# Kernel tuning notes

Measured on AMD Instinct MI355X. Metric: run time of the kernel, lower is better.

## Reference

```python
import jax, jax.numpy as jnp
import numpy as np

BS, N, C = 16, 128, 512
EPS = 1e-5


def setup_inputs() -> dict:
    key = jax.random.key(0)
    ks = jax.random.split(key, 6)
    x = jax.random.normal(ks[0], (BS, N, C), dtype=jnp.float32)
    y = jax.random.normal(ks[1], (BS, C), dtype=jnp.float32)
    # edge conv: Conv2d(2C -> 1, 1x1), init std sqrt(2/(1*1*1))
    conv_e_w = jax.random.normal(ks[2], (1, 2 * C), dtype=jnp.float32) * np.sqrt(2.0)
    conv_e_b = jnp.zeros((1,), dtype=jnp.float32)
    bn_e_g = jnp.ones((1,), dtype=jnp.float32)
    bn_e_b = jnp.zeros((1,), dtype=jnp.float32)
    bn_e_m = jnp.zeros((1,), dtype=jnp.float32)
    bn_e_v = jnp.ones((1,), dtype=jnp.float32)
    # feature conv: Conv2d(2C -> C, 1x1), init std sqrt(2/C)
    conv_f_w = jax.random.normal(ks[3], (C, 2 * C), dtype=jnp.float32) * np.sqrt(2.0 / C)
    conv_f_b = jnp.zeros((C,), dtype=jnp.float32)
    bn_f_g = jnp.ones((C,), dtype=jnp.float32)
    bn_f_b = jnp.zeros((C,), dtype=jnp.float32)
    bn_f_m = jnp.zeros((C,), dtype=jnp.float32)
    bn_f_v = jnp.ones((C,), dtype=jnp.float32)
    return {
        "x": x, "y": y,
        "conv_e_w": conv_e_w, "conv_e_b": conv_e_b,
        "bn_e_g": bn_e_g, "bn_e_b": bn_e_b, "bn_e_m": bn_e_m, "bn_e_v": bn_e_v,
        "conv_f_w": conv_f_w, "conv_f_b": conv_f_b,
        "bn_f_g": bn_f_g, "bn_f_b": bn_f_b, "bn_f_m": bn_f_m, "bn_f_v": bn_f_v,
    }


def reference(x, y, conv_e_w, conv_e_b, bn_e_g, bn_e_b, bn_e_m, bn_e_v,
              conv_f_w, conv_f_b, bn_f_g, bn_f_b, bn_f_m, bn_f_v):
    bs, n, c = x.shape
    # ---- Wcompute: pairwise |x_i - x_j| -> conv1x1(2C->1) + BN + mask + softmax ----
    diff = jnp.abs(x[:, :, None, :] - x[:, None, :, :])  # [bs, N, N, C]
    w_diff = conv_e_w[0, :c]   # weights on pairwise-diff channels
    w_y = conv_e_w[0, c:]      # weights on broadcast y channels
    # 1x1 conv collapses to einsum; y part is constant over (i, j)
    score = (jnp.einsum('bijc,c->bij', diff, w_diff)
             + (y @ w_y)[:, None, None] + conv_e_b[0])  # [bs, N, N]
    # BatchNorm2d(1), inference mode
    score = (score - bn_e_m[0]) * (bn_e_g[0] * jax.lax.rsqrt(bn_e_v[0] + EPS)) + bn_e_b[0]
    # mask diagonal (W_id * 1e8) then softmax over neighbors j
    score = score - jnp.eye(n, dtype=score.dtype)[None] * 1e8
    W = jax.nn.softmax(score, axis=2)  # [bs, N, N]
    # ---- Gconv: neighbor aggregation + conv1x1(2C->C) + BN + ReLU ----
    x_nb = jnp.einsum('bij,bjc->bic', W, x)       # [bs, N, C]
    h = jnp.concatenate([x, x_nb], axis=2)        # [bs, N, 2C]
    out = jnp.einsum('bnk,ck->bnc', h, conv_f_w) + conv_f_b  # [bs, N, C]
    # BatchNorm2d(C), inference mode (per-channel)
    out = (out - bn_f_m) * (bn_f_g * jax.lax.rsqrt(bn_f_v + EPS)) + bn_f_b
    return jax.nn.relu(out)
```

## Files before the change

kernel.cpp:

```cpp
#include <hip/hip_runtime.h>
#include <hip/hip_bf16.h>

#define BSZ  16
#define NTOK 128
#define CHN  512
#define KTOT 1024
#define EPSV 1e-5f

typedef __attribute__((ext_vector_type(8))) short bf16x8;
typedef __attribute__((ext_vector_type(4))) float f32x4;

union BfPack4 { ushort4 u; __hip_bfloat16 h[4]; };

__global__ __launch_bounds__(128)
void k1_score_softmax_xnb(const float* __restrict__ xg,
                          const float* __restrict__ wde,
                          const float* __restrict__ bn_e_g,
                          const float* __restrict__ bn_e_v,
                          const float* __restrict__ wf,
                          __hip_bfloat16* __restrict__ hb,
                          __hip_bfloat16* __restrict__ wfb)
{
    __shared__ float xs[64][129];
    __shared__ float wrow[4][132];
    __shared__ float red[2][8];

    const int t   = threadIdx.x;
    const int blk = blockIdx.x;
    const int b   = blk >> 5;
    const int i0  = (blk & 31) << 2;
    const float* __restrict__ xb = xg + (size_t)b * NTOK * CHN;

    {
        const float* wr = wf + (size_t)blk * KTOT;
        float4 u0 = *(const float4*)&wr[t * 8];
        float4 u1 = *(const float4*)&wr[t * 8 + 4];
        BfPack4 p0, p1;
        p0.h[0] = __float2bfloat16(u0.x); p0.h[1] = __float2bfloat16(u0.y);
        p0.h[2] = __float2bfloat16(u0.z); p0.h[3] = __float2bfloat16(u0.w);
        p1.h[0] = __float2bfloat16(u1.x); p1.h[1] = __float2bfloat16(u1.y);
        p1.h[2] = __float2bfloat16(u1.z); p1.h[3] = __float2bfloat16(u1.w);
        *(ushort4*)&wfb[(size_t)blk * KTOT + t * 8]     = p0.u;
        *(ushort4*)&wfb[(size_t)blk * KTOT + t * 8 + 4] = p1.u;
    }

    float acc[4] = {0.f, 0.f, 0.f, 0.f};

    for (int c0 = 0; c0 < CHN; c0 += 64) {
        #pragma unroll
        for (int p = 0; p < 16; ++p) {
            const int j  = p * 8 + (t >> 4);
            const int c4 = (t & 15) * 4;
            float4 v = *(const float4*)&xb[(size_t)j * CHN + c0 + c4];
            xs[c4 + 0][j] = v.x; xs[c4 + 1][j] = v.y;
            xs[c4 + 2][j] = v.z; xs[c4 + 3][j] = v.w;
        }
        __syncthreads();

        #pragma unroll 4
        for (int g4 = 0; g4 < 16; ++g4) {
            const int c = c0 + g4 * 4;
            const float4 wdv = *(const float4*)&wde[c];
            const float4 xi0 = *(const float4*)&xb[(size_t)(i0 + 0) * CHN + c];
            const float4 xi1 = *(const float4*)&xb[(size_t)(i0 + 1) * CHN + c];
            const float4 xi2 = *(const float4*)&xb[(size_t)(i0 + 2) * CHN + c];
            const float4 xi3 = *(const float4*)&xb[(size_t)(i0 + 3) * CHN + c];
            const int cl = g4 * 4;
            const float xj0 = xs[cl + 0][t];
            const float xj1 = xs[cl + 1][t];
            const float xj2 = xs[cl + 2][t];
            const float xj3 = xs[cl + 3][t];
            acc[0] += fabsf(xi0.x - xj0) * wdv.x + fabsf(xi0.y - xj1) * wdv.y
                    + fabsf(xi0.z - xj2) * wdv.z + fabsf(xi0.w - xj3) * wdv.w;
            acc[1] += fabsf(xi1.x - xj0) * wdv.x + fabsf(xi1.y - xj1) * wdv.y
                    + fabsf(xi1.z - xj2) * wdv.z + fabsf(xi1.w - xj3) * wdv.w;
            acc[2] += fabsf(xi2.x - xj0) * wdv.x + fabsf(xi2.y - xj1) * wdv.y
                    + fabsf(xi2.z - xj2) * wdv.z + fabsf(xi2.w - xj3) * wdv.w;
            acc[3] += fabsf(xi3.x - xj0) * wdv.x + fabsf(xi3.y - xj1) * wdv.y
                    + fabsf(xi3.z - xj2) * wdv.z + fabsf(xi3.w - xj3) * wdv.w;
        }
        __syncthreads();
    }

    const float sc = bn_e_g[0] * rsqrtf(bn_e_v[0] + EPSV);
    float logit[4];
    #pragma unroll
    for (int ti = 0; ti < 4; ++ti) {
        logit[ti] = acc[ti] * sc;
        if (t == i0 + ti) logit[ti] -= 1e8f;
    }
    const int wid = t >> 6, lane = t & 63;
    float mx[4];
    #pragma unroll
    for (int ti = 0; ti < 4; ++ti) {
        float v = logit[ti];
        #pragma unroll
        for (int off = 32; off > 0; off >>= 1) v = fmaxf(v, __shfl_xor(v, off));
        mx[ti] = v;
    }
    if (lane == 0) {
        red[wid][0] = mx[0]; red[wid][1] = mx[1];
        red[wid][2] = mx[2]; red[wid][3] = mx[3];
    }
    __syncthreads();
    float pe[4], sm[4];
    #pragma unroll
    for (int ti = 0; ti < 4; ++ti) {
        const float M = fmaxf(red[0][ti], red[1][ti]);
        pe[ti] = __expf(logit[ti] - M);
        float v = pe[ti];
        #pragma unroll
        for (int off = 32; off > 0; off >>= 1) v += __shfl_xor(v, off);
        sm[ti] = v;
    }
    if (lane == 0) {
        red[wid][4] = sm[0]; red[wid][5] = sm[1];
        red[wid][6] = sm[2]; red[wid][7] = sm[3];
    }
    __syncthreads();
    #pragma unroll
    for (int ti = 0; ti < 4; ++ti) {
        const float S = red[0][4 + ti] + red[1][4 + ti];
        wrow[ti][t] = pe[ti] / S;
    }
    __syncthreads();

    const int c4 = t << 2;
    float4 av[4];
    #pragma unroll
    for (int ti = 0; ti < 4; ++ti) { av[ti].x = av[ti].y = av[ti].z = av[ti].w = 0.f; }

    for (int j = 0; j < NTOK; ++j) {
        const float4 xj = *(const float4*)&xb[(size_t)j * CHN + c4];
        const float w0 = wrow[0][j], w1 = wrow[1][j], w2 = wrow[2][j], w3 = wrow[3][j];
        av[0].x += w0 * xj.x; av[0].y += w0 * xj.y; av[0].z += w0 * xj.z; av[0].w += w0 * xj.w;
        av[1].x += w1 * xj.x; av[1].y += w1 * xj.y; av[1].z += w1 * xj.z; av[1].w += w1 * xj.w;
        av[2].x += w2 * xj.x; av[2].y += w2 * xj.y; av[2].z += w2 * xj.z; av[2].w += w2 * xj.w;
        av[3].x += w3 * xj.x; av[3].y += w3 * xj.y; av[3].z += w3 * xj.z; av[3].w += w3 * xj.w;
    }

    #pragma unroll
    for (int ti = 0; ti < 4; ++ti) {
        const size_t row = (size_t)(b * NTOK + i0 + ti);
        BfPack4 pk;
        pk.h[0] = __float2bfloat16(av[ti].x); pk.h[1] = __float2bfloat16(av[ti].y);
        pk.h[2] = __float2bfloat16(av[ti].z); pk.h[3] = __float2bfloat16(av[ti].w);
        *(ushort4*)&hb[row * KTOT + CHN + c4] = pk.u;
        const float4 xv = *(const float4*)&xb[(size_t)(i0 + ti) * CHN + c4];
        pk.h[0] = __float2bfloat16(xv.x); pk.h[1] = __float2bfloat16(xv.y);
        pk.h[2] = __float2bfloat16(xv.z); pk.h[3] = __float2bfloat16(xv.w);
        *(ushort4*)&hb[row * KTOT + c4] = pk.u;
    }
}

__global__ __launch_bounds__(256)
void k2_gemm_bn_relu(const __hip_bfloat16* __restrict__ hbp,
                     const __hip_bfloat16* __restrict__ wfbp,
                     const float* __restrict__ fb,
                     const float* __restrict__ gg,
                     const float* __restrict__ bb,
                     const float* __restrict__ mm,
                     const float* __restrict__ vv,
                     float* __restrict__ out)
{
    const int blk  = blockIdx.x;
    const int r0   = (blk >> 3) << 6;
    const int c0   = (blk & 7) << 6;
    const int t    = threadIdx.x;
    const int w    = t >> 6;
    const int lane = t & 63;
    const int wm   = w & 1;
    const int wn   = w >> 1;
    const int m16  = lane & 15;
    const int q    = lane >> 4;

    const short* A0 = (const short*)hbp  + (size_t)(r0 + wm * 32 + m16) * KTOT + q * 8;
    const short* B0 = (const short*)wfbp + (size_t)(c0 + wn * 32 + m16) * KTOT + q * 8;

    f32x4 acc00 = {0.f, 0.f, 0.f, 0.f};
    f32x4 acc01 = acc00, acc10 = acc00, acc11 = acc00;

    #pragma unroll 4
    for (int k0 = 0; k0 < KTOT; k0 += 32) {
        const bf16x8 aA = *(const bf16x8*)(A0 + k0);
        const bf16x8 aB = *(const bf16x8*)(A0 + 16 * KTOT + k0);
        const bf16x8 bA = *(const bf16x8*)(B0 + k0);
        const bf16x8 bB = *(const bf16x8*)(B0 + 16 * KTOT + k0);
        acc00 = __builtin_amdgcn_mfma_f32_16x16x32_bf16(aA, bA, acc00, 0, 0, 0);
        acc01 = __builtin_amdgcn_mfma_f32_16x16x32_bf16(aA, bB, acc01, 0, 0, 0);
        acc10 = __builtin_amdgcn_mfma_f32_16x16x32_bf16(aB, bA, acc10, 0, 0, 0);
        acc11 = __builtin_amdgcn_mfma_f32_16x16x32_bf16(aB, bB, acc11, 0, 0, 0);
    }

    #pragma unroll
    for (int ni = 0; ni < 2; ++ni) {
        const int c = c0 + wn * 32 + ni * 16 + m16;
        const float gf = gg[c] * rsqrtf(vv[c] + EPSV);
        const float ad = fb[c] - mm[c];
        const float bv = bb[c];
        const f32x4 acr0 = ni ? acc01 : acc00;
        const f32x4 acr1 = ni ? acc11 : acc10;
        #pragma unroll
        for (int r2 = 0; r2 < 4; ++r2) {
            int row = r0 + wm * 32 + q * 4 + r2;
            float val = (acr0[r2] + ad) * gf + bv;
            out[(size_t)row * CHN + c] = fmaxf(val, 0.f);
            row += 16;
            val = (acr1[r2] + ad) * gf + bv;
            out[(size_t)row * CHN + c] = fmaxf(val, 0.f);
        }
    }
}

extern "C" void kernel_launch(void* const* d_in, const int* in_sizes, int n_in,
                              void* d_out, int out_size, void* d_ws, size_t ws_size,
                              hipStream_t stream) {
    const float* x        = (const float*)d_in[0];
    const float* conv_e_w = (const float*)d_in[2];
    const float* bn_e_g   = (const float*)d_in[4];
    const float* bn_e_v   = (const float*)d_in[7];
    const float* conv_f_w = (const float*)d_in[8];
    const float* conv_f_b = (const float*)d_in[9];
    const float* bn_f_g   = (const float*)d_in[10];
    const float* bn_f_b   = (const float*)d_in[11];
    const float* bn_f_m   = (const float*)d_in[12];
    const float* bn_f_v   = (const float*)d_in[13];
    float* out = (float*)d_out;

    __hip_bfloat16* hb  = (__hip_bfloat16*)d_ws;
    __hip_bfloat16* wfb = hb + (size_t)2048 * 1024;

    k1_score_softmax_xnb<<<512, 128, 0, stream>>>(x, conv_e_w, bn_e_g, bn_e_v,
                                                  conv_f_w, hb, wfb);
    k2_gemm_bn_relu<<<256, 256, 0, stream>>>(hb, wfb, conv_f_b, bn_f_g, bn_f_b,
                                             bn_f_m, bn_f_v, out);
}
```

Measured before the change: 141.6 us.

## Split channel reduction across four thread groups in score kernel with 512 threads

The first kernel grows from 128 to 512 threads per block. The pairwise score reduction over channels is split into four channel quarters, each staged into its own shared-memory slab, and the partials are combined through shared memory before the softmax. The neighbor aggregation is likewise split over four j-quarters and summed through shared memory. This gives each block more waves to hide memory latency and shortens the serial loop per thread, at the cost of more shared memory, extra barriers and partial-sum traffic. The softmax section places __syncthreads calls inside divergent branches, with matching counts on each side.

After: 153.5 us. 8.4% more time.

```diff
diff --git a/kernel.cpp b/kernel.cpp
--- a/kernel.cpp
+++ b/kernel.cpp
@@ -7,12 +7,15 @@
 #define KTOT 1024
 #define EPSV 1e-5f
 
+#define LROW 132
+#define QS   (32 * LROW)
+
 typedef __attribute__((ext_vector_type(8))) short bf16x8;
 typedef __attribute__((ext_vector_type(4))) float f32x4;
 
 union BfPack4 { ushort4 u; __hip_bfloat16 h[4]; };
 
-__global__ __launch_bounds__(128)
+__global__ __launch_bounds__(512, 4)
 void k1_score_softmax_xnb(const float* __restrict__ xg,
                           const float* __restrict__ wde,
                           const float* __restrict__ bn_e_g,
@@ -21,9 +24,10 @@
                           __hip_bfloat16* __restrict__ hb,
                           __hip_bfloat16* __restrict__ wfb)
 {
-    __shared__ float xs[64][129];
-    __shared__ float wrow[4][132];
-    __shared__ float red[2][8];
+    __shared__ float smem[4 * QS];
+    __shared__ float part[4][4][128];
+    __shared__ float wrow[4][LROW];
+    __shared__ float red[16];
 
     const int t   = threadIdx.x;
     const int blk = blockIdx.x;
@@ -31,122 +35,154 @@
     const int i0  = (blk & 31) << 2;
     const float* __restrict__ xb = xg + (size_t)b * NTOK * CHN;
 
-    {
+    if (t < 256) {
         const float* wr = wf + (size_t)blk * KTOT;
-        float4 u0 = *(const float4*)&wr[t * 8];
-        float4 u1 = *(const float4*)&wr[t * 8 + 4];
-        BfPack4 p0, p1;
-        p0.h[0] = __float2bfloat16(u0.x); p0.h[1] = __float2bfloat16(u0.y);
-        p0.h[2] = __float2bfloat16(u0.z); p0.h[3] = __float2bfloat16(u0.w);
-        p1.h[0] = __float2bfloat16(u1.x); p1.h[1] = __float2bfloat16(u1.y);
-        p1.h[2] = __float2bfloat16(u1.z); p1.h[3] = __float2bfloat16(u1.w);
-        *(ushort4*)&wfb[(size_t)blk * KTOT + t * 8]     = p0.u;
-        *(ushort4*)&wfb[(size_t)blk * KTOT + t * 8 + 4] = p1.u;
-    }
-
+        float4 u = *(const float4*)&wr[t * 4];
+        BfPack4 p;
+        p.h[0] = __float2bfloat16(u.x); p.h[1] = __float2bfloat16(u.y);
+        p.h[2] = __float2bfloat16(u.z); p.h[3] = __float2bfloat16(u.w);
+        *(ushort4*)&wfb[(size_t)blk * KTOT + t * 4] = p.u;
+    }
+
+    const int j = t & 127;
+    const int q = t >> 7;
     float acc[4] = {0.f, 0.f, 0.f, 0.f};
 
-    for (int c0 = 0; c0 < CHN; c0 += 64) {
-        #pragma unroll
-        for (int p = 0; p < 16; ++p) {
-            const int j  = p * 8 + (t >> 4);
-            const int c4 = (t & 15) * 4;
-            float4 v = *(const float4*)&xb[(size_t)j * CHN + c0 + c4];
-            xs[c4 + 0][j] = v.x; xs[c4 + 1][j] = v.y;
-            xs[c4 + 2][j] = v.z; xs[c4 + 3][j] = v.w;
-        }
-        __syncthreads();
-
-        #pragma unroll 4
-        for (int g4 = 0; g4 < 16; ++g4) {
-            const int c = c0 + g4 * 4;
-            const float4 wdv = *(const float4*)&wde[c];
+    const int j_s = t >> 2;
+    const int lg  = t & 3;
+
+    for (int s = 0; s < 4; ++s) {
+        #pragma unroll
+        for (int g = 0; g < 8; ++g) {
+            const int G   = lg + 4 * g;
+            const int qq  = G >> 3;
+            const int idx = G & 7;
+            const int cg  = qq * 128 + s * 32 + idx * 4;
+            float4 v = *(const float4*)&xb[(size_t)j_s * CHN + cg];
+            float* dst = &smem[qq * QS + (idx * 4) * LROW + j_s];
+            dst[0 * LROW] = v.x; dst[1 * LROW] = v.y;
+            dst[2 * LROW] = v.z; dst[3 * LROW] = v.w;
+        }
+        __syncthreads();
+
+        const int cbase = q * 128 + s * 32;
+        #pragma unroll
+        for (int g = 0; g < 8; ++g) {
+            const int c = cbase + g * 4;
+            const float4 wd  = *(const float4*)&wde[c];
             const float4 xi0 = *(const float4*)&xb[(size_t)(i0 + 0) * CHN + c];
             const float4 xi1 = *(const float4*)&xb[(size_t)(i0 + 1) * CHN + c];
             const float4 xi2 = *(const float4*)&xb[(size_t)(i0 + 2) * CHN + c];
             const float4 xi3 = *(const float4*)&xb[(size_t)(i0 + 3) * CHN + c];
-            const int cl = g4 * 4;
-            const float xj0 = xs[cl + 0][t];
-            const float xj1 = xs[cl + 1][t];
-            const float xj2 = xs[cl + 2][t];
-            const float xj3 = xs[cl + 3][t];
-            acc[0] += fabsf(xi0.x - xj0) * wdv.x + fabsf(xi0.y - xj1) * wdv.y
-                    + fabsf(xi0.z - xj2) * wdv.z + fabsf(xi0.w - xj3) * wdv.w;
-            acc[1] += fabsf(xi1.x - xj0) * wdv.x + fabsf(xi1.y - xj1) * wdv.y
-                    + fabsf(xi1.z - xj2) * wdv.z + fabsf(xi1.w - xj3) * wdv.w;
-            acc[2] += fabsf(xi2.x - xj0) * wdv.x + fabsf(xi2.y - xj1) * wdv.y
-                    + fabsf(xi2.z - xj2) * wdv.z + fabsf(xi2.w - xj3) * wdv.w;
-            acc[3] += fabsf(xi3.x - xj0) * wdv.x + fabsf(xi3.y - xj1) * wdv.y
-                    + fabsf(xi3.z - xj2) * wdv.z + fabsf(xi3.w - xj3) * wdv.w;
-        }
-        __syncthreads();
-    }
-
-    const float sc = bn_e_g[0] * rsqrtf(bn_e_v[0] + EPSV);
-    float logit[4];
-    #pragma unroll
-    for (int ti = 0; ti < 4; ++ti) {
-        logit[ti] = acc[ti] * sc;
-        if (t == i0 + ti) logit[ti] -= 1e8f;
-    }
-    const int wid = t >> 6, lane = t & 63;
-    float mx[4];
-    #pragma unroll
-    for (int ti = 0; ti < 4; ++ti) {
-        float v = logit[ti];
-        #pragma unroll
-        for (int off = 32; off > 0; off >>= 1) v = fmaxf(v, __shfl_xor(v, off));
-        mx[ti] = v;
-    }
-    if (lane == 0) {
-        red[wid][0] = mx[0]; red[wid][1] = mx[1];
-        red[wid][2] = mx[2]; red[wid][3] = mx[3];
-    }
+            const float* xr = &smem[q * QS + (g * 4) * LROW + j];
+            const float xj0 = xr[0 * LROW];
+            const float xj1 = xr[1 * LROW];
+            const float xj2 = xr[2 * LROW];
+            const float xj3 = xr[3 * LROW];
+            acc[0] += fabsf(xi0.x - xj0) * wd.x + fabsf(xi0.y - xj1) * wd.y
+                    + fabsf(xi0.z - xj2) * wd.z + fabsf(xi0.w - xj3) * wd.w;
+            acc[1] += fabsf(xi1.x - xj0) * wd.x + fabsf(xi1.y - xj1) * wd.y
+                    + fabsf(xi1.z - xj2) * wd.z + fabsf(xi1.w - xj3) * wd.w;
+            acc[2] += fabsf(xi2.x - xj0) * wd.x + fabsf(xi2.y - xj1) * wd.y
+                    + fabsf(xi2.z - xj2) * wd.z + fabsf(xi2.w - xj3) * wd.w;
+            acc[3] += fabsf(xi3.x - xj0) * wd.x + fabsf(xi3.y - xj1) * wd.y
+                    + fabsf(xi3.z - xj2) * wd.z + fabsf(xi3.w - xj3) * wd.w;
+        }
+        __syncthreads();
+    }
+
+    #pragma unroll
+    for (int ti = 0; ti < 4; ++ti) part[q][ti][j] = acc[ti];
     __syncthreads();
-    float pe[4], sm[4];
-    #pragma unroll
-    for (int ti = 0; ti < 4; ++ti) {
-        const float M = fmaxf(red[0][ti], red[1][ti]);
-        pe[ti] = __expf(logit[ti] - M);
-        float v = pe[ti];
-        #pragma unroll
-        for (int off = 32; off > 0; off >>= 1) v += __shfl_xor(v, off);
-        sm[ti] = v;
-    }
-    if (lane == 0) {
-        red[wid][4] = sm[0]; red[wid][5] = sm[1];
-        red[wid][6] = sm[2]; red[wid][7] = sm[3];
+
+    if (t < 128) {
+        const float sc = bn_e_g[0] * rsqrtf(bn_e_v[0] + EPSV);
+        float logit[4];
+        #pragma unroll
+        for (int ti = 0; ti < 4; ++ti) {
+            logit[ti] = (part[0][ti][t] + part[1][ti][t]
+                       + part[2][ti][t] + part[3][ti][t]) * sc;
+            if (t == i0 + ti) logit[ti] -= 1e8f;
+        }
+        const int wid = t >> 6, lane = t & 63;
+        float mx[4];
+        #pragma unroll
+        for (int ti = 0; ti < 4; ++ti) {
+            float v = logit[ti];
+            #pragma unroll
+            for (int off = 32; off > 0; off >>= 1) v = fmaxf(v, __shfl_xor(v, off));
+            mx[ti] = v;
+        }
+        if (lane == 0) {
+            red[wid * 8 + 0] = mx[0]; red[wid * 8 + 1] = mx[1];
+            red[wid * 8 + 2] = mx[2]; red[wid * 8 + 3] = mx[3];
+        }
+        __syncthreads();
+        float pe[4], sm[4];
+        #pragma unroll
+        for (int ti = 0; ti < 4; ++ti) {
+            const float M = fmaxf(red[ti], red[8 + ti]);
+            pe[ti] = __expf(logit[ti] - M);
+            float v = pe[ti];
+            #pragma unroll
+            for (int off = 32; off > 0; off >>= 1) v += __shfl_xor(v, off);
+            sm[ti] = v;
+        }
+        if (lane == 0) {
+            red[wid * 8 + 4] = sm[0]; red[wid * 8 + 5] = sm[1];
+            red[wid * 8 + 6] = sm[2]; red[wid * 8 + 7] = sm[3];
+        }
+        __syncthreads();
+        #pragma unroll
+        for (int ti = 0; ti < 4; ++ti) {
+            const float S = red[4 + ti] + red[12 + ti];
+            wrow[ti][t] = pe[ti] / S;
+        }
+    } else {
+        __syncthreads();
+        __syncthreads();
     }
     __syncthreads();
-    #pragma unroll
-    for (int ti = 0; ti < 4; ++ti) {
-        const float S = red[0][4 + ti] + red[1][4 + ti];
-        wrow[ti][t] = pe[ti] / S;
-    }
+
+    const int c4 = (t & 127) << 2;
+    const int jq = t >> 7;
+    float4 a2[4];
+    #pragma unroll
+    for (int ti = 0; ti < 4; ++ti) { a2[ti].x = a2[ti].y = a2[ti].z = a2[ti].w = 0.f; }
+
+    #pragma unroll 4
+    for (int jj = 0; jj < 32; ++jj) {
+        const int jx = jq * 32 + jj;
+        const float4 xj = *(const float4*)&xb[(size_t)jx * CHN + c4];
+        const float w0 = wrow[0][jx], w1 = wrow[1][jx];
+        const float w2 = wrow[2][jx], w3 = wrow[3][jx];
+        a2[0].x += w0 * xj.x; a2[0].y += w0 * xj.y; a2[0].z += w0 * xj.z; a2[0].w += w0 * xj.w;
+        a2[1].x += w1 * xj.x; a2[1].y += w1 * xj.y; a2[1].z += w1 * xj.z; a2[1].w += w1 * xj.w;
+        a2[2].x += w2 * xj.x; a2[2].y += w2 * xj.y; a2[2].z += w2 * xj.z; a2[2].w += w2 * xj.w;
+        a2[3].x += w3 * xj.x; a2[3].y += w3 * xj.y; a2[3].z += w3 * xj.z; a2[3].w += w3 * xj.w;
+    }
+    #pragma unroll
+    for (int ti = 0; ti < 4; ++ti)
+        *(float4*)&smem[(jq * 4 + ti) * CHN + c4] = a2[ti];
     __syncthreads();
 
-    const int c4 = t << 2;
-    float4 av[4];
-    #pragma unroll
-    for (int ti = 0; ti < 4; ++ti) { av[ti].x = av[ti].y = av[ti].z = av[ti].w = 0.f; }
-
-    for (int j = 0; j < NTOK; ++j) {
-        const float4 xj = *(const float4*)&xb[(size_t)j * CHN + c4];
-        const float w0 = wrow[0][j], w1 = wrow[1][j], w2 = wrow[2][j], w3 = wrow[3][j];
-        av[0].x += w0 * xj.x; av[0].y += w0 * xj.y; av[0].z += w0 * xj.z; av[0].w += w0 * xj.w;
-        av[1].x += w1 * xj.x; av[1].y += w1 * xj.y; av[1].z += w1 * xj.z; av[1].w += w1 * xj.w;
-        av[2].x += w2 * xj.x; av[2].y += w2 * xj.y; av[2].z += w2 * xj.z; av[2].w += w2 * xj.w;
-        av[3].x += w3 * xj.x; av[3].y += w3 * xj.y; av[3].z += w3 * xj.z; av[3].w += w3 * xj.w;
-    }
-
-    #pragma unroll
-    for (int ti = 0; ti < 4; ++ti) {
-        const size_t row = (size_t)(b * NTOK + i0 + ti);
+    {
+        const int ti2 = t >> 7;
+        float4 s0 = *(const float4*)&smem[(0 * 4 + ti2) * CHN + c4];
+        float4 s1 = *(const float4*)&smem[(1 * 4 + ti2) * CHN + c4];
+        float4 s2 = *(const float4*)&smem[(2 * 4 + ti2) * CHN + c4];
+        float4 s3 = *(const float4*)&smem[(3 * 4 + ti2) * CHN + c4];
+        float4 sum;
+        sum.x = s0.x + s1.x + s2.x + s3.x;
+        sum.y = s0.y + s1.y + s2.y + s3.y;
+        sum.z = s0.z + s1.z + s2.z + s3.z;
+        sum.w = s0.w + s1.w + s2.w + s3.w;
+        const size_t row = (size_t)(b * NTOK + i0 + ti2);
         BfPack4 pk;
-        pk.h[0] = __float2bfloat16(av[ti].x); pk.h[1] = __float2bfloat16(av[ti].y);
-        pk.h[2] = __float2bfloat16(av[ti].z); pk.h[3] = __float2bfloat16(av[ti].w);
+        pk.h[0] = __float2bfloat16(sum.x); pk.h[1] = __float2bfloat16(sum.y);
+        pk.h[2] = __float2bfloat16(sum.z); pk.h[3] = __float2bfloat16(sum.w);
         *(ushort4*)&hb[row * KTOT + CHN + c4] = pk.u;
-        const float4 xv = *(const float4*)&xb[(size_t)(i0 + ti) * CHN + c4];
+        const float4 xv = *(const float4*)&xb[(size_t)(i0 + ti2) * CHN + c4];
         pk.h[0] = __float2bfloat16(xv.x); pk.h[1] = __float2bfloat16(xv.y);
         pk.h[2] = __float2bfloat16(xv.z); pk.h[3] = __float2bfloat16(xv.w);
         *(ushort4*)&hb[row * KTOT + c4] = pk.u;
@@ -172,10 +208,10 @@
     const int wm   = w & 1;
     const int wn   = w >> 1;
     const int m16  = lane & 15;
-    const int q    = lane >> 4;
-
-    const short* A0 = (const short*)hbp  + (size_t)(r0 + wm * 32 + m16) * KTOT + q * 8;
-    const short* B0 = (const short*)wfbp + (size_t)(c0 + wn * 32 + m16) * KTOT + q * 8;
+    const int qq   = lane >> 4;
+
+    const short* A0 = (const short*)hbp  + (size_t)(r0 + wm * 32 + m16) * KTOT + qq * 8;
+    const short* B0 = (const short*)wfbp + (size_t)(c0 + wn * 32 + m16) * KTOT + qq * 8;
 
     f32x4 acc00 = {0.f, 0.f, 0.f, 0.f};
     f32x4 acc01 = acc00, acc10 = acc00, acc11 = acc00;
@@ -202,7 +238,7 @@
         const f32x4 acr1 = ni ? acc11 : acc10;
         #pragma unroll
         for (int r2 = 0; r2 < 4; ++r2) {
-            int row = r0 + wm * 32 + q * 4 + r2;
+            int row = r0 + wm * 32 + qq * 4 + r2;
             float val = (acr0[r2] + ad) * gf + bv;
             out[(size_t)row * CHN + c] = fmaxf(val, 0.f);
             row += 16;
@@ -230,7 +266,7 @@
     __hip_bfloat16* hb  = (__hip_bfloat16*)d_ws;
     __hip_bfloat16* wfb = hb + (size_t)2048 * 1024;
 
-    k1_score_softmax_xnb<<<512, 128, 0, stream>>>(x, conv_e_w, bn_e_g, bn_e_v,
+    k1_score_softmax_xnb<<<512, 512, 0, stream>>>(x, conv_e_w, bn_e_g, bn_e_v,
                                                   conv_f_w, hb, wfb);
     k2_gemm_bn_relu<<<256, 256, 0, stream>>>(hb, wfb, conv_f_b, bn_f_g, bn_f_b,
                                              bn_f_m, bn_f_v, out);
```

## Split score kernel into transpose, split-K scores, softmax, and MFMA aggregation

Applied to the files above, without the earlier changes.

Replaces the single fused score/softmax/aggregation kernel with four kernels. A transpose kernel writes x^T in fp32 and bf16. The pairwise score is split across 8 channel slices (4096 blocks) to raise parallelism, with partial sums written to a workspace and then reduced in a softmax kernel. The neighbor aggregation W·x now runs on MFMA in bf16. This adds extra launches, global round-trips for partial scores, and lower precision in W and x for the aggregation.

Result: faster. 123.1 us (median of 3 runs) (-13.1%).

```diff
diff --git a/kernel.cpp b/kernel.cpp
--- a/kernel.cpp
+++ b/kernel.cpp
@@ -1,7 +1,6 @@
 #include <hip/hip_runtime.h>
 #include <hip/hip_bf16.h>
 
-#define BSZ  16
 #define NTOK 128
 #define CHN  512
 #define KTOT 1024
@@ -12,144 +11,206 @@
 
 union BfPack4 { ushort4 u; __hip_bfloat16 h[4]; };
 
+
+__global__ __launch_bounds__(256)
+void k0_transpose(const float* __restrict__ xg,
+                  float* __restrict__ xT,
+                  __hip_bfloat16* __restrict__ xTbf,
+                  __hip_bfloat16* __restrict__ hb)
+{
+    __shared__ float ts[64 * 68];
+    const int t  = threadIdx.x;
+    const int bk = blockIdx.x;
+    const int b  = bk >> 4;
+    const int jt = (bk >> 3) & 1;
+    const int ct = bk & 7;
+    const int j0 = jt * 64, c0 = ct * 64;
+
+    const int jr = t >> 2, qd = t & 3;
+    const float* src = xg + ((size_t)(b * NTOK) + j0 + jr) * CHN + c0 + qd * 16;
+    float4 v0 = *(const float4*)&src[0];
+    float4 v1 = *(const float4*)&src[4];
+    float4 v2 = *(const float4*)&src[8];
+    float4 v3 = *(const float4*)&src[12];
+    *(float4*)&ts[jr * 68 + qd * 16 + 0]  = v0;
+    *(float4*)&ts[jr * 68 + qd * 16 + 4]  = v1;
+    *(float4*)&ts[jr * 68 + qd * 16 + 8]  = v2;
+    *(float4*)&ts[jr * 68 + qd * 16 + 12] = v3;
+
+    {
+        __hip_bfloat16* hrow = hb + ((size_t)(b * NTOK) + j0 + jr) * KTOT + c0 + qd * 16;
+        BfPack4 p;
+        p.h[0]=__float2bfloat16(v0.x); p.h[1]=__float2bfloat16(v0.y);
+        p.h[2]=__float2bfloat16(v0.z); p.h[3]=__float2bfloat16(v0.w);
+        *(ushort4*)&hrow[0] = p.u;
+        p.h[0]=__float2bfloat16(v1.x); p.h[1]=__float2bfloat16(v1.y);
+        p.h[2]=__float2bfloat16(v1.z); p.h[3]=__float2bfloat16(v1.w);
+        *(ushort4*)&hrow[4] = p.u;
+        p.h[0]=__float2bfloat16(v2.x); p.h[1]=__float2bfloat16(v2.y);
+        p.h[2]=__float2bfloat16(v2.z); p.h[3]=__float2bfloat16(v2.w);
+        *(ushort4*)&hrow[8] = p.u;
+        p.h[0]=__float2bfloat16(v3.x); p.h[1]=__float2bfloat16(v3.y);
+        p.h[2]=__float2bfloat16(v3.z); p.h[3]=__float2bfloat16(v3.w);
+        *(ushort4*)&hrow[12] = p.u;
+    }
+    __syncthreads();
+
+    const int cs = t >> 4, jj = (t & 15) * 4;
+    #pragma unroll
+    for (int m = 0; m < 4; ++m) {
+        const int c = cs + 16 * m;
+        float4 o;
+        o.x = ts[(jj + 0) * 68 + c];
+        o.y = ts[(jj + 1) * 68 + c];
+        o.z = ts[(jj + 2) * 68 + c];
+        o.w = ts[(jj + 3) * 68 + c];
+        const size_t base = ((size_t)(b * CHN) + c0 + c) * NTOK + j0 + jj;
+        *(float4*)&xT[base] = o;
+        BfPack4 p;
+        p.h[0]=__float2bfloat16(o.x); p.h[1]=__float2bfloat16(o.y);
+        p.h[2]=__float2bfloat16(o.z); p.h[3]=__float2bfloat16(o.w);
+        *(ushort4*)&xTbf[base] = p.u;
+    }
+}
+
 __global__ __launch_bounds__(128)
-void k1_score_softmax_xnb(const float* __restrict__ xg,
-                          const float* __restrict__ wde,
-                          const float* __restrict__ bn_e_g,
-                          const float* __restrict__ bn_e_v,
-                          const float* __restrict__ wf,
-                          __hip_bfloat16* __restrict__ hb,
-                          __hip_bfloat16* __restrict__ wfb)
-{
-    __shared__ float xs[64][129];
-    __shared__ float wrow[4][132];
-    __shared__ float red[2][8];
-
-    const int t   = threadIdx.x;
-    const int blk = blockIdx.x;
-    const int b   = blk >> 5;
-    const int i0  = (blk & 31) << 2;
-    const float* __restrict__ xb = xg + (size_t)b * NTOK * CHN;
+void k1a_scores(const float* __restrict__ xg,
+                const float* __restrict__ xT,
+                const float* __restrict__ wde,
+                float* __restrict__ part)
+{
+    const int bk = blockIdx.x;
+    const int s  = bk & 7;
+    const int iq = (bk >> 3) & 31;
+    const int b  = bk >> 8;
+    const int i0 = iq * 4;
+    const int c0 = s * 64;
+    const int j  = threadIdx.x;
+
+    const float* xtp = xT + ((size_t)(b * CHN) + c0) * NTOK + j;
+    const float* xip = xg + ((size_t)(b * NTOK) + i0) * CHN + c0;
+
+    float acc0 = 0.f, acc1 = 0.f, acc2 = 0.f, acc3 = 0.f;
+
+    #pragma unroll 2
+    for (int cc = 0; cc < 64; cc += 8) {
+        float xj[8];
+        #pragma unroll
+        for (int k = 0; k < 8; ++k) xj[k] = xtp[(cc + k) * NTOK];
+        #pragma unroll
+        for (int k = 0; k < 8; ++k) {
+            const int c = cc + k;
+            const float wd  = wde[c0 + c];
+            const float xi0 = xip[0 * CHN + c];
+            const float xi1 = xip[1 * CHN + c];
+            const float xi2 = xip[2 * CHN + c];
+            const float xi3 = xip[3 * CHN + c];
+            acc0 += fabsf(xi0 - xj[k]) * wd;
+            acc1 += fabsf(xi1 - xj[k]) * wd;
+            acc2 += fabsf(xi2 - xj[k]) * wd;
+            acc3 += fabsf(xi3 - xj[k]) * wd;
+        }
+    }
+
+    float* pp = part + ((size_t)s * 16 + b) * (NTOK * NTOK) + (size_t)i0 * NTOK + j;
+    pp[0 * NTOK] = acc0;
+    pp[1 * NTOK] = acc1;
+    pp[2 * NTOK] = acc2;
+    pp[3 * NTOK] = acc3;
+}
+
+__global__ __launch_bounds__(128)
+void k1b_softmax(const float* __restrict__ part,
+                 const float* __restrict__ bn_e_g,
+                 const float* __restrict__ bn_e_v,
+                 __hip_bfloat16* __restrict__ Wbf)
+{
+    const int bk = blockIdx.x;
+    const int b  = bk >> 6;
+    const int i  = (bk & 63) * 2 + (threadIdx.x >> 6);
+    const int l  = threadIdx.x & 63;
+
+    const float* pp = part + (size_t)(b * NTOK + i) * NTOK;
+    float p1 = 0.f, p2 = 0.f;
+    #pragma unroll
+    for (int s = 0; s < 8; ++s) {
+        p1 += pp[(size_t)s * 16 * NTOK * NTOK + l];
+        p2 += pp[(size_t)s * 16 * NTOK * NTOK + l + 64];
+    }
+    const float sc = bn_e_g[0] * rsqrtf(bn_e_v[0] + EPSV);
+    float l1 = p1 * sc - (l == i ? 1e8f : 0.f);
+    float l2 = p2 * sc - (l + 64 == i ? 1e8f : 0.f);
+
+    float m = fmaxf(l1, l2);
+    #pragma unroll
+    for (int off = 32; off > 0; off >>= 1) m = fmaxf(m, __shfl_xor(m, off));
+    const float e1 = __expf(l1 - m);
+    const float e2 = __expf(l2 - m);
+    float ssum = e1 + e2;
+    #pragma unroll
+    for (int off = 32; off > 0; off >>= 1) ssum += __shfl_xor(ssum, off);
+    const float inv = 1.f / ssum;
+
+    __hip_bfloat16* wr = Wbf + (size_t)(b * NTOK + i) * NTOK;
+    wr[l]      = __float2bfloat16(e1 * inv);
+    wr[l + 64] = __float2bfloat16(e2 * inv);
+}
+
+__global__ __launch_bounds__(256)
+void k1c_xnb(const __hip_bfloat16* __restrict__ Wbf,
+             const __hip_bfloat16* __restrict__ xTbf,
+             const float* __restrict__ wf,
+             __hip_bfloat16* __restrict__ hb,
+             __hip_bfloat16* __restrict__ wfb)
+{
+    const int bk = blockIdx.x;
+    const int t  = threadIdx.x;
 
     {
-        const float* wr = wf + (size_t)blk * KTOT;
-        float4 u0 = *(const float4*)&wr[t * 8];
-        float4 u1 = *(const float4*)&wr[t * 8 + 4];
-        BfPack4 p0, p1;
-        p0.h[0] = __float2bfloat16(u0.x); p0.h[1] = __float2bfloat16(u0.y);
-        p0.h[2] = __float2bfloat16(u0.z); p0.h[3] = __float2bfloat16(u0.w);
-        p1.h[0] = __float2bfloat16(u1.x); p1.h[1] = __float2bfloat16(u1.y);
-        p1.h[2] = __float2bfloat16(u1.z); p1.h[3] = __float2bfloat16(u1.w);
-        *(ushort4*)&wfb[(size_t)blk * KTOT + t * 8]     = p0.u;
-        *(ushort4*)&wfb[(size_t)blk * KTOT + t * 8 + 4] = p1.u;
-    }
-
-    float acc[4] = {0.f, 0.f, 0.f, 0.f};
-
-    for (int c0 = 0; c0 < CHN; c0 += 64) {
+        const float* wr = wf + (size_t)bk * KTOT;
+        float4 u = *(const float4*)&wr[t * 4];
+        BfPack4 p;
+        p.h[0]=__float2bfloat16(u.x); p.h[1]=__float2bfloat16(u.y);
+        p.h[2]=__float2bfloat16(u.z); p.h[3]=__float2bfloat16(u.w);
+        *(ushort4*)&wfb[(size_t)bk * KTOT + t * 4] = p.u;
+    }
+
+    const int b  = bk >> 5;
+    const int mt = (bk >> 3) & 3;
+    const int ct = bk & 7;
+    const int i0 = mt * 32, c0 = ct * 64;
+
+    const int w    = t >> 6;
+    const int lane = t & 63;
+    const int wm   = w & 1;
+    const int wn   = w >> 1;
+    const int m16  = lane & 15;
+    const int q    = lane >> 4;
+
+    const short* A0 = (const short*)Wbf  + (size_t)(b * NTOK + i0 + wm * 16 + m16) * NTOK + q * 8;
+    const short* B0 = (const short*)xTbf + ((size_t)(b * CHN) + c0 + wn * 32 + m16) * NTOK + q * 8;
+
+    f32x4 acc0 = {0.f, 0.f, 0.f, 0.f};
+    f32x4 acc1 = acc0;
+
+    #pragma unroll
+    for (int k0 = 0; k0 < NTOK; k0 += 32) {
+        const bf16x8 a  = *(const bf16x8*)(A0 + k0);
+        const bf16x8 b0 = *(const bf16x8*)(B0 + k0);
+        const bf16x8 b1 = *(const bf16x8*)(B0 + 16 * NTOK + k0);
+        acc0 = __builtin_amdgcn_mfma_f32_16x16x32_bf16(a, b0, acc0, 0, 0, 0);
+        acc1 = __builtin_amdgcn_mfma_f32_16x16x32_bf16(a, b1, acc1, 0, 0, 0);
+    }
+
+    #pragma unroll
+    for (int ni = 0; ni < 2; ++ni) {
+        const int c = c0 + wn * 32 + ni * 16 + m16;
+        const f32x4 ac = ni ? acc1 : acc0;
         #pragma unroll
-        for (int p = 0; p < 16; ++p) {
-            const int j  = p * 8 + (t >> 4);
-            const int c4 = (t & 15) * 4;
-            float4 v = *(const float4*)&xb[(size_t)j * CHN + c0 + c4];
-            xs[c4 + 0][j] = v.x; xs[c4 + 1][j] = v.y;
-            xs[c4 + 2][j] = v.z; xs[c4 + 3][j] = v.w;
+        for (int r = 0; r < 4; ++r) {
+            const int i = i0 + wm * 16 + q * 4 + r;
+            hb[(size_t)(b * NTOK + i) * KTOT + CHN + c] = __float2bfloat16(ac[r]);
         }
-        __syncthreads();
-
-        #pragma unroll 4
-        for (int g4 = 0; g4 < 16; ++g4) {
-            const int c = c0 + g4 * 4;
-            const float4 wdv = *(const float4*)&wde[c];
-            const float4 xi0 = *(const float4*)&xb[(size_t)(i0 + 0) * CHN + c];
-            const float4 xi1 = *(const float4*)&xb[(size_t)(i0 + 1) * CHN + c];
-            const float4 xi2 = *(const float4*)&xb[(size_t)(i0 + 2) * CHN + c];
-            const float4 xi3 = *(const float4*)&xb[(size_t)(i0 + 3) * CHN + c];
-            const int cl = g4 * 4;
-            const float xj0 = xs[cl + 0][t];
-            const float xj1 = xs[cl + 1][t];
-            const float xj2 = xs[cl + 2][t];
-            const float xj3 = xs[cl + 3][t];
-            acc[0] += fabsf(xi0.x - xj0) * wdv.x + fabsf(xi0.y - xj1) * wdv.y
-                    + fabsf(xi0.z - xj2) * wdv.z + fabsf(xi0.w - xj3) * wdv.w;
-            acc[1] += fabsf(xi1.x - xj0) * wdv.x + fabsf(xi1.y - xj1) * wdv.y
-                    + fabsf(xi1.z - xj2) * wdv.z + fabsf(xi1.w - xj3) * wdv.w;
-            acc[2] += fabsf(xi2.x - xj0) * wdv.x + fabsf(xi2.y - xj1) * wdv.y
-                    + fabsf(xi2.z - xj2) * wdv.z + fabsf(xi2.w - xj3) * wdv.w;
-            acc[3] += fabsf(xi3.x - xj0) * wdv.x + fabsf(xi3.y - xj1) * wdv.y
-                    + fabsf(xi3.z - xj2) * wdv.z + fabsf(xi3.w - xj3) * wdv.w;
-        }
-        __syncthreads();
-    }
-
-    const float sc = bn_e_g[0] * rsqrtf(bn_e_v[0] + EPSV);
-    float logit[4];
-    #pragma unroll
-    for (int ti = 0; ti < 4; ++ti) {
-        logit[ti] = acc[ti] * sc;
-        if (t == i0 + ti) logit[ti] -= 1e8f;
-    }
-    const int wid = t >> 6, lane = t & 63;
-    float mx[4];
-    #pragma unroll
-    for (int ti = 0; ti < 4; ++ti) {
-        float v = logit[ti];
-        #pragma unroll
-        for (int off = 32; off > 0; off >>= 1) v = fmaxf(v, __shfl_xor(v, off));
-        mx[ti] = v;
-    }
-    if (lane == 0) {
-        red[wid][0] = mx[0]; red[wid][1] = mx[1];
-        red[wid][2] = mx[2]; red[wid][3] = mx[3];
-    }
-    __syncthreads();
-    float pe[4], sm[4];
-    #pragma unroll
-    for (int ti = 0; ti < 4; ++ti) {
-        const float M = fmaxf(red[0][ti], red[1][ti]);
-        pe[ti] = __expf(logit[ti] - M);
-        float v = pe[ti];
-        #pragma unroll
-        for (int off = 32; off > 0; off >>= 1) v += __shfl_xor(v, off);
-        sm[ti] = v;
-    }
-    if (lane == 0) {
-        red[wid][4] = sm[0]; red[wid][5] = sm[1];
-        red[wid][6] = sm[2]; red[wid][7] = sm[3];
-    }
-    __syncthreads();
-    #pragma unroll
-    for (int ti = 0; ti < 4; ++ti) {
-        const float S = red[0][4 + ti] + red[1][4 + ti];
-        wrow[ti][t] = pe[ti] / S;
-    }
-    __syncthreads();
-
-    const int c4 = t << 2;
-    float4 av[4];
-    #pragma unroll
-    for (int ti = 0; ti < 4; ++ti) { av[ti].x = av[ti].y = av[ti].z = av[ti].w = 0.f; }
-
-    for (int j = 0; j < NTOK; ++j) {
-        const float4 xj = *(const float4*)&xb[(size_t)j * CHN + c4];
-        const float w0 = wrow[0][j], w1 = wrow[1][j], w2 = wrow[2][j], w3 = wrow[3][j];
-        av[0].x += w0 * xj.x; av[0].y += w0 * xj.y; av[0].z += w0 * xj.z; av[0].w += w0 * xj.w;
-        av[1].x += w1 * xj.x; av[1].y += w1 * xj.y; av[1].z += w1 * xj.z; av[1].w += w1 * xj.w;
-        av[2].x += w2 * xj.x; av[2].y += w2 * xj.y; av[2].z += w2 * xj.z; av[2].w += w2 * xj.w;
-        av[3].x += w3 * xj.x; av[3].y += w3 * xj.y; av[3].z += w3 * xj.z; av[3].w += w3 * xj.w;
-    }
-
-    #pragma unroll
-    for (int ti = 0; ti < 4; ++ti) {
-        const size_t row = (size_t)(b * NTOK + i0 + ti);
-        BfPack4 pk;
-        pk.h[0] = __float2bfloat16(av[ti].x); pk.h[1] = __float2bfloat16(av[ti].y);
-        pk.h[2] = __float2bfloat16(av[ti].z); pk.h[3] = __float2bfloat16(av[ti].w);
-        *(ushort4*)&hb[row * KTOT + CHN + c4] = pk.u;
-        const float4 xv = *(const float4*)&xb[(size_t)(i0 + ti) * CHN + c4];
-        pk.h[0] = __float2bfloat16(xv.x); pk.h[1] = __float2bfloat16(xv.y);
-        pk.h[2] = __float2bfloat16(xv.z); pk.h[3] = __float2bfloat16(xv.w);
-        *(ushort4*)&hb[row * KTOT + c4] = pk.u;
     }
 }
 
@@ -172,10 +233,10 @@
     const int wm   = w & 1;
     const int wn   = w >> 1;
     const int m16  = lane & 15;
-    const int q    = lane >> 4;
-
-    const short* A0 = (const short*)hbp  + (size_t)(r0 + wm * 32 + m16) * KTOT + q * 8;
-    const short* B0 = (const short*)wfbp + (size_t)(c0 + wn * 32 + m16) * KTOT + q * 8;
+    const int qq   = lane >> 4;
+
+    const short* A0 = (const short*)hbp  + (size_t)(r0 + wm * 32 + m16) * KTOT + qq * 8;
+    const short* B0 = (const short*)wfbp + (size_t)(c0 + wn * 32 + m16) * KTOT + qq * 8;
 
     f32x4 acc00 = {0.f, 0.f, 0.f, 0.f};
     f32x4 acc01 = acc00, acc10 = acc00, acc11 = acc00;
@@ -202,7 +263,7 @@
         const f32x4 acr1 = ni ? acc11 : acc10;
         #pragma unroll
         for (int r2 = 0; r2 < 4; ++r2) {
-            int row = r0 + wm * 32 + q * 4 + r2;
+            int row = r0 + wm * 32 + qq * 4 + r2;
             float val = (acr0[r2] + ad) * gf + bv;
             out[(size_t)row * CHN + c] = fmaxf(val, 0.f);
             row += 16;
@@ -227,11 +288,18 @@
     const float* bn_f_v   = (const float*)d_in[13];
     float* out = (float*)d_out;
 
-    __hip_bfloat16* hb  = (__hip_bfloat16*)d_ws;
-    __hip_bfloat16* wfb = hb + (size_t)2048 * 1024;
-
-    k1_score_softmax_xnb<<<512, 128, 0, stream>>>(x, conv_e_w, bn_e_g, bn_e_v,
-                                                  conv_f_w, hb, wfb);
+    char* ws = (char*)d_ws;
+    float*           xT   = (float*)(ws);
+    float*           part = (float*)(ws + (4u << 20));
+    __hip_bfloat16*  hb   = (__hip_bfloat16*)(ws + (12u << 20));
+    __hip_bfloat16*  wfb  = (__hip_bfloat16*)(ws + (16u << 20));
+    __hip_bfloat16*  Wbf  = (__hip_bfloat16*)(ws + (17u << 20));
+    __hip_bfloat16*  xTbf = (__hip_bfloat16*)(ws + (17u << 20) + (512u << 10));
+
+    k0_transpose<<<256, 256, 0, stream>>>(x, xT, xTbf, hb);
+    k1a_scores<<<4096, 128, 0, stream>>>(x, xT, conv_e_w, part);
+    k1b_softmax<<<1024, 128, 0, stream>>>(part, bn_e_g, bn_e_v, Wbf);
+    k1c_xnb<<<512, 256, 0, stream>>>(Wbf, xTbf, conv_f_w, hb, wfb);
     k2_gemm_bn_relu<<<256, 256, 0, stream>>>(hb, wfb, conv_f_b, bn_f_g, bn_f_b,
                                              bn_f_m, bn_f_v, out);
 }
```
